# Performance work log

Measured on AMD Instinct MI355X. Metric: run time of the kernel, lower is better.

## Reference

```python
import jax, jax.numpy as jnp
import numpy as np

B, M, DIM, HID, GRID, IMG = 32, 4096, 768, 128, 15, 240
P = GRID * GRID
NL, TOPK, BETA, EPS = 3, 10, 1.0, 1e-5


def setup_inputs() -> dict:
    key = jax.random.key(0)
    ks = jax.random.split(key, 12)
    r = lambda k, s: jax.random.normal(k, s, jnp.float32) * 0.02
    H2 = HID // 2
    return dict(
        query_tokens=jax.random.normal(ks[0], (B, P, DIM), jnp.float32),
        prompt_tokens=jax.random.normal(ks[1], (B, M, DIM), jnp.float32),
        layer_idx=0,
        sbn_g=jnp.ones((NL, DIM)), sbn_b=jnp.zeros((NL, DIM)),
        sbn_m=jnp.zeros((NL, DIM)), sbn_v=jnp.ones((NL, DIM)),
        w1=r(ks[2], (HID, DIM, 3, 3)),
        bn1_g=jnp.ones(HID), bn1_b=jnp.zeros(HID), bn1_m=jnp.zeros(HID), bn1_v=jnp.ones(HID),
        wt1=r(ks[3], (HID, HID, 2, 2)), bt1=jnp.zeros(HID),
        w2=r(ks[4], (H2, HID, 3, 3)),
        bn2_g=jnp.ones(H2), bn2_b=jnp.zeros(H2), bn2_m=jnp.zeros(H2), bn2_v=jnp.ones(H2),
        wt2=r(ks[5], (H2, H2, 2, 2)), bt2=jnp.zeros(H2),
        w3=r(ks[6], (2, H2, 1, 1)), b3=jnp.zeros(2),
        g1=r(ks[7], (HID, DIM)),
        gbn1_g=jnp.ones(HID), gbn1_b=jnp.zeros(HID), gbn1_m=jnp.zeros(HID), gbn1_v=jnp.ones(HID),
        g2=r(ks[8], (H2, HID)),
        gbn2_g=jnp.ones(H2), gbn2_b=jnp.zeros(H2), gbn2_m=jnp.zeros(H2), gbn2_v=jnp.ones(H2),
        g3=r(ks[9], (2, H2)),
    )


def _conv(x, w, pad):
    return jax.lax.conv_general_dilated(x, w, (1, 1), [(pad, pad), (pad, pad)],
                                        dimension_numbers=('NCHW', 'OIHW', 'NCHW'))


def _convT2(x, w, b):
    # ConvTranspose2d(k=2, s=2): non-overlapping -> einsum + depth-to-space
    Bn, C, H, W = x.shape
    O = w.shape[1]
    y = jnp.einsum('bchw,coij->bohiwj', x, w).reshape(Bn, O, H * 2, W * 2)
    return y + b[None, :, None, None]


def _bn2(x, g, b, m, v):
    s = g / jnp.sqrt(v + EPS)
    return (x - m[:, None, None]) * s[:, None, None] + b[:, None, None]


def _bn1(x, g, b, m, v):
    return (x - m) * (g / jnp.sqrt(v + EPS)) + b


def reference(query_tokens, prompt_tokens, layer_idx, sbn_g, sbn_b, sbn_m, sbn_v,
              w1, bn1_g, bn1_b, bn1_m, bn1_v, wt1, bt1,
              w2, bn2_g, bn2_b, bn2_m, bn2_v, wt2, bt2, w3, b3,
              g1, gbn1_g, gbn1_b, gbn1_m, gbn1_v,
              g2, gbn2_g, gbn2_b, gbn2_m, gbn2_v, g3):
    # --- align_prompt_to_query ---
    qn = query_tokens / jnp.maximum(jnp.linalg.norm(query_tokens, axis=-1, keepdims=True), 1e-12)
    pn = prompt_tokens / jnp.maximum(jnp.linalg.norm(prompt_tokens, axis=-1, keepdims=True), 1e-12)
    sim = jnp.einsum('bpd,bmd->bpm', qn, pn)            # [B,P,M]
    indices = jnp.argmax(sim, axis=-1)                  # [B,P]
    max_sim = jnp.max(sim, axis=-1)
    aligned = jnp.take_along_axis(prompt_tokens, indices[..., None], axis=1)  # [B,P,D]
    residual_map = 0.5 * (1.0 - max_sim)
    context = query_tokens + BETA * jnp.abs(query_tokens - aligned)
    # --- seg head ---
    li = min(int(layer_idx), NL - 1)
    cm = context.transpose(0, 2, 1).reshape(B, DIM, GRID, GRID)
    cm = _bn2(cm, sbn_g[li], sbn_b[li], sbn_m[li], sbn_v[li])
    h = jax.nn.relu(_bn2(_conv(cm, w1, 1), bn1_g, bn1_b, bn1_m, bn1_v))
    h = _convT2(h, wt1, bt1)                            # 15 -> 30
    h = jax.nn.relu(_bn2(_conv(h, w2, 1), bn2_g, bn2_b, bn2_m, bn2_v))
    h = _convT2(h, wt2, bt2)                            # 30 -> 60
    low = _conv(h, w3, 0) + b3[None, :, None, None]     # [B,2,60,60]
    seg = jax.image.resize(low, (B, 2, IMG, IMG), method='bilinear')  # align_corners=False
    patch_map = jax.nn.softmax(low, axis=1)[:, 1].reshape(B, -1)
    # --- global head: avg pool + topk-residual pool ---
    avg_pool = context.mean(axis=1)
    _, ti = jax.lax.top_k(residual_map, TOPK)
    topk_tokens = jnp.take_along_axis(context, ti[..., None], axis=1).mean(axis=1)
    pooled = 0.5 * avg_pool + 0.5 * topk_tokens
    g = jax.nn.relu(_bn1(pooled @ g1.T, gbn1_g, gbn1_b, gbn1_m, gbn1_v))
    g = jax.nn.relu(_bn1(g @ g2.T, gbn2_g, gbn2_b, gbn2_m, gbn2_v))
    gl = g @ g3.T
    logit = gl[:, 1] - gl[:, 0]
    return (seg, gl, logit, jax.nn.sigmoid(logit), patch_map, residual_map, context, aligned, indices)
```

## Files before the change

### kernel.cpp

```cpp
#include <hip/hip_runtime.h>
#include <cmath>

#define EPSC 1e-5f
typedef unsigned short ushortT;
typedef unsigned int uintT;
typedef __attribute__((ext_vector_type(8))) short bf16x8;
typedef __attribute__((ext_vector_type(4))) float f32x4;

constexpr size_t O_SEG   = 0;
constexpr size_t O_GL    = 3686400;
constexpr size_t O_LOGIT = 3686464;
constexpr size_t O_PROB  = 3686496;
constexpr size_t O_PATCH = 3686528;
constexpr size_t O_RES   = 3801728;
constexpr size_t O_CTX   = 3808928;
constexpr size_t O_ALN   = 9338528;
constexpr size_t O_IDX   = 14868128;

constexpr size_t WS_MS64 = 0;
constexpr size_t WS_AVG  = 14400;
constexpr size_t CB      = 38976;
constexpr size_t WS_QPK  = CB;
constexpr size_t WS_TOP2G= CB + 5898240;
constexpr size_t WS_CPH  = CB;
constexpr size_t WS_CPL  = CB + 3551232;
constexpr size_t WS_WPK  = CB + 7102464;
constexpr size_t WS_H1   = CB + 8000000;
constexpr size_t WS_T1H  = CB;
constexpr size_t WS_T1L  = CB + 2097152;
constexpr size_t WS_H2   = CB + 4200000;
constexpr size_t WS_T2   = CB + 6050000;
constexpr size_t WS_WPK2 = CB + 8950000;
constexpr size_t WS_LOW  = CB;

__global__ __launch_bounds__(256) void k_qpack(const float* __restrict__ Q,
                                               ushortT* __restrict__ qpk) {
  int id = blockIdx.x * 256 + threadIdx.x;
  int r = id & 15;
  int g = (id >> 4) & 3;
  int rest = id >> 6;
  int sub = rest % 15;
  int bkc = rest / 15;
  int kc = bkc % 24, b = bkc / 24;
  if (b >= 32) return;
  int q = sub * 16 + r;
  int k0 = kc * 32 + g * 8;
  float x[8];
  if (q < 225) {
    const float* src = Q + ((size_t)(b * 225 + q)) * 768 + k0;
#pragma unroll
    for (int e = 0; e < 8; ++e) x[e] = src[e];
  } else {
#pragma unroll
    for (int e = 0; e < 8; ++e) x[e] = 0.f;
  }
  uintT hb[8];
#pragma unroll
  for (int e = 0; e < 8; ++e) hb[e] = __float_as_uint(x[e]);
  uint4 hv;
  hv.x = (hb[0] >> 16) | (hb[1] & 0xFFFF0000u);
  hv.y = (hb[2] >> 16) | (hb[3] & 0xFFFF0000u);
  hv.z = (hb[4] >> 16) | (hb[5] & 0xFFFF0000u);
  hv.w = (hb[6] >> 16) | (hb[7] & 0xFFFF0000u);
  size_t base = ((size_t)(b * 24 + kc) * 30 + sub) * 512 + (g * 16 + r) * 8;
  *(uint4*)(qpk + base) = hv;
}

__global__ __launch_bounds__(256, 3) void k_simm(const ushortT* __restrict__ qpk,
    const float* __restrict__ PM, float4* __restrict__ top2g) {
  __shared__ ushortT sP[2 * 2048];
  __shared__ float4 smrg[240];
  __shared__ float srp[64];
  int sp = blockIdx.x, b = blockIdx.y;
  int t = threadIdx.x;
  int w = t >> 6, l = t & 63;
  int mq = t >> 3, kq = t & 7;
  const int sub0 = w * 4;
  const ushortT* qB0 = qpk + (size_t)(b * 24) * 30 * 512;

#define LOADQ(KC)                                                             \
  {                                                                           \
    const ushortT* qk = qB0 + (size_t)(KC) * (30 * 512);                      \
    _Pragma("unroll")                                                         \
    for (int ss = 0; ss < 4; ++ss) {                                          \
      int subc = sub0 + ss; if (subc > 14) subc = 14;                         \
      qh[ss] = *(const bf16x8*)(qk + subc * 512 + l * 8);                     \
    }                                                                         \
  }

#define LOADP(PR, KC)                                                         \
  {                                                                           \
    _Pragma("unroll")                                                         \
    for (int pass = 0; pass < 2; ++pass) {                                    \
      int ml = mq + pass * 32;                                                \
      PR[pass] = *(const float4*)(pmBase + (size_t)ml * 768 + (KC) * 32 + kq * 4); \
    }                                                                         \
  }

#define CVTW(PR, BUF)                                                         \
  {                                                                           \
    _Pragma("unroll")                                                         \
    for (int pass = 0; pass < 2; ++pass) {                                    \
      int ml = mq + pass * 32;                                                \
      float4 x = PR[pass];                                                    \
      pn[pass] += x.x * x.x + x.y * x.y + x.z * x.z + x.w * x.w;              \
      uintT a0 = __float_as_uint(x.x), a1 = __float_as_uint(x.y);             \
      uintT a2 = __float_as_uint(x.z), a3 = __float_as_uint(x.w);             \
      uintT h01 = (a0 >> 16) | (a1 & 0xFFFF0000u);                            \
      uintT h23 = (a2 >> 16) | (a3 & 0xFFFF0000u);                            \
      int off = (ml >> 4) * 512 + (kq >> 1) * 128 + (ml & 15) * 8 + (kq & 1) * 4; \
      *(uint2*)(&sP[(BUF) + off]) = make_uint2(h01, h23);                     \
    }                                                                         \
  }

#define MFMAPH(BUF)                                                           \
  {                                                                           \
    bf16x8 bh[4];                                                             \
    _Pragma("unroll")                                                         \
    for (int mm = 0; mm < 4; ++mm)                                            \
      bh[mm] = *(const bf16x8*)&sP[(BUF) + mm * 512 + l * 8];                 \
    _Pragma("unroll")                                                         \
    for (int ss = 0; ss < 4; ++ss) {                                          \
      if (sub0 + ss < 15) {                                                   \
        _Pragma("unroll")                                                     \
        for (int mm = 0; mm < 4; ++mm) {                                      \
          acc[ss][mm] = __builtin_amdgcn_mfma_f32_16x16x32_bf16(              \
              qh[ss], bh[mm], acc[ss][mm], 0, 0, 0);                          \
        }                                                                     \
      }                                                                       \
    }                                                                         \
  }

  f32x4 acc[4][4];
#pragma unroll
  for (int ss = 0; ss < 4; ++ss)
#pragma unroll
    for (int mm = 0; mm < 4; ++mm) acc[ss][mm] = (f32x4){0.f, 0.f, 0.f, 0.f};
  float pn[2] = {0.f, 0.f};
  const int mbase = sp * 64;
  const float* pmBase = PM + ((size_t)b * 4096 + mbase) * 768;

  bf16x8 qh[4];
  float4 pr[2];

  LOADP(pr, 0);
  CVTW(pr, 0);
  __syncthreads();

  for (int kc2 = 0; kc2 < 12; ++kc2) {
    int kc = kc2 * 2;
    LOADQ(kc);
    LOADP(pr, kc + 1);
    MFMAPH(0);
    CVTW(pr, 2048);
    __syncthreads();
    LOADQ(kc + 1);
    if (kc2 < 11) {
      LOADP(pr, kc + 2);
    }
    MFMAPH(2048);
    if (kc2 < 11) {
      CVTW(pr, 0);
    }
    __syncthreads();
  }

#pragma unroll
  for (int pass = 0; pass < 2; ++pass) {
    float v = pn[pass];
    v += __shfl_xor(v, 1); v += __shfl_xor(v, 2); v += __shfl_xor(v, 4);
    if (kq == 0) srp[mq + pass * 32] = 1.0f / fmaxf(sqrtf(v), 1e-12f);
  }
  __syncthreads();
  float rpv_[4];
#pragma unroll
  for (int mf = 0; mf < 4; ++mf) rpv_[mf] = srp[mf * 16 + (l & 15)];
#pragma unroll
  for (int ss = 0; ss < 4; ++ss) {
    int sub = sub0 + ss;
    if (sub >= 15) break;
#pragma unroll
    for (int j = 0; j < 4; ++j) {
      float a1 = -1e30f, a2 = -1e30f; int ai1 = -1, ai2 = -1;
#pragma unroll
      for (int mf = 0; mf < 4; ++mf) {
        float v = acc[ss][mf][j] * rpv_[mf];
        int mi = mbase + mf * 16 + (l & 15);
        if (v > a1) { a2 = a1; ai2 = ai1; a1 = v; ai1 = mi; }
        else if (v > a2) { a2 = v; ai2 = mi; }
      }
#pragma unroll
      for (int o = 1; o <= 8; o <<= 1) {
        float b1 = __shfl_xor(a1, o), b2 = __shfl_xor(a2, o);
        int bi1 = __shfl_xor(ai1, o), bi2 = __shfl_xor(ai2, o);
        if (b1 > a1) {
          float n2; int ni2;
          if (a1 > b2) { n2 = a1; ni2 = ai1; } else { n2 = b2; ni2 = bi2; }
          a1 = b1; ai1 = bi1; a2 = n2; ai2 = ni2;
        } else {
          if (b1 > a2) { a2 = b1; ai2 = bi1; }
        }
      }
      if ((l & 15) == j) {
        int row = sub * 16 + (l >> 4) * 4 + j;
        smrg[row] = make_float4(a1, a2, __int_as_float(ai1), __int_as_float(ai2));
      }
    }
  }
  __syncthreads();
  if (t < 240) top2g[((size_t)(b * 240 + t)) * 64 + sp] = smrg[t];
#undef LOADQ
#undef LOADP
#undef CVTW
#undef MFMAPH
}

__global__ __launch_bounds__(256) void k_refine(const float* __restrict__ Q,
    const float* __restrict__ PM, const float4* __restrict__ top2g,
    float* __restrict__ oIdx, float* __restrict__ oRes,
    float* __restrict__ oCtx, float* __restrict__ oAln,
    double* __restrict__ ms64) {
  int wid = (blockIdx.x * 256 + threadIdx.x) >> 6;
  int lane = threadIdx.x & 63;
  if (wid >= 7200) return;
  int b = wid / 225, pr = wid % 225;
  float4 e = top2g[((size_t)(b * 240 + pr)) * 64 + lane];
  float v1 = e.x, v2 = e.y;
  int i1 = __float_as_int(e.z), i2 = __float_as_int(e.w);
  int cand[8];
#pragma unroll
  for (int k = 0; k < 8; ++k) {
    float v = v1; int mi = i1;
    if (v2 > v || (v2 == v && (uintT)i2 < (uintT)mi)) { v = v2; mi = i2; }
#pragma unroll
    for (int o = 1; o <= 32; o <<= 1) {
      float ov = __shfl_xor(v, o); int omi = __shfl_xor(mi, o);
      if (ov > v || (ov == v && (uintT)omi < (uintT)mi)) { v = ov; mi = omi; }
    }
    cand[k] = mi;
    if (i1 == mi) v1 = -3e38f;
    if (i2 == mi) v2 = -3e38f;
  }
  const float* qr = Q + ((size_t)b * 225 + pr) * 768;
  float qv[12]; double nq = 0.0;
#pragma unroll
  for (int j = 0; j < 12; ++j) { float x = qr[lane + 64 * j]; qv[j] = x; nq += (double)x * (double)x; }
#pragma unroll
  for (int o = 1; o < 64; o <<= 1) nq += __shfl_xor(nq, o);
  double qn = fmax(sqrt(nq), 1e-12);
  double best = -1e300; int bi = 0;
#pragma unroll
  for (int pass = 0; pass < 2; ++pass) {
    const float* pp[4];
    double d[4], nn[4];
#pragma unroll
    for (int c = 0; c < 4; ++c) {
      pp[c] = PM + ((size_t)b * 4096 + cand[pass * 4 + c]) * 768 + lane;
      d[c] = 0.0; nn[c] = 0.0;
    }
#pragma unroll
    for (int j = 0; j < 12; ++j) {
#pragma unroll
      for (int c = 0; c < 4; ++c) {
        double pe = (double)pp[c][64 * j];
        d[c] += (double)qv[j] * pe;
        nn[c] += pe * pe;
      }
    }
#pragma unroll
    for (int o = 1; o < 64; o <<= 1) {
#pragma unroll
      for (int c = 0; c < 4; ++c) {
        d[c] += __shfl_xor(d[c], o);
        nn[c] += __shfl_xor(nn[c], o);
      }
    }
#pragma unroll
    for (int c = 0; c < 4; ++c) {
      int mi = cand[pass * 4 + c];
      double s = d[c] / (qn * fmax(sqrt(nn[c]), 1e-12));
      if (s > best || (s == best && mi < bi)) { best = s; bi = mi; }
    }
  }
  if (lane == 0) {
    oIdx[wid] = (float)bi;
    oRes[wid] = (float)(0.5 * (1.0 - best));
    ms64[wid] = best;
  }
  const float* ar = PM + ((size_t)b * 4096 + bi) * 768;
  float* cw = oCtx + (size_t)wid * 768;
  float* aw = oAln + (size_t)wid * 768;
#pragma unroll
  for (int j = 0; j < 12; ++j) {
    float a = ar[lane + 64 * j];
    float qq = qv[j];
    aw[lane + 64 * j] = a;
    cw[lane + 64 * j] = qq + fabsf(qq - a);
  }
}

__global__ __launch_bounds__(256) void k_pool(const float* __restrict__ ctx,
                                              float* __restrict__ avg) {
  int b = blockIdx.x, c = blockIdx.y, t = threadIdx.x;
  int d = c * 256 + t;
  float s = 0.f;
  for (int p = 0; p < 225; ++p) s += ctx[((size_t)b * 225 + p) * 768 + d];
  avg[b * 768 + d] = s / 225.0f;
}

__global__ __launch_bounds__(256) void k_head(const float* __restrict__ ctx,
    const double* __restrict__ ms64, const float* __restrict__ avg,
    const float* __restrict__ g1, const float* __restrict__ b1g, const float* __restrict__ b1b,
    const float* __restrict__ b1m, const float* __restrict__ b1v,
    const float* __restrict__ g2, const float* __restrict__ b2g, const float* __restrict__ b2b,
    const float* __restrict__ b2m, const float* __restrict__ b2v,
    const float* __restrict__ g3,
    float* __restrict__ oGl, float* __restrict__ oLogit, float* __restrict__ oProb) {
  __shared__ int tki[10];
  __shared__ float pooled[768];
  __shared__ float h1s[128];
  __shared__ float h2s[64];
  __shared__ float gls[2];
  int b = blockIdx.x, t = threadIdx.x;
  if (t < 64) {
    double rv[4]; int ri[4];
#pragma unroll
    for (int j = 0; j < 4; ++j) {
      int p = t + 64 * j; ri[j] = p;
      rv[j] = (p < 225) ? 0.5 * (1.0 - ms64[b * 225 + p]) : -1e300;
    }
    for (int k = 0; k < 10; ++k) {
      double bv = -1e301; int bI = 1 << 30;
#pragma unroll
      for (int j = 0; j < 4; ++j)
        if (rv[j] > bv || (rv[j] == bv && ri[j] < bI)) { bv = rv[j]; bI = ri[j]; }
#pragma unroll
      for (int o = 1; o < 64; o <<= 1) {
        double ov = __shfl_xor(bv, o); int oi = __shfl_xor(bI, o);
        if (ov > bv || (ov == bv && oi < bI)) { bv = ov; bI = oi; }
      }
      if (t == 0) tki[k] = bI;
#pragma unroll
      for (int j = 0; j < 4; ++j) if (ri[j] == bI) rv[j] = -1e300;
    }
  }
  __syncthreads();
#pragma unroll
  for (int di = 0; di < 3; ++di) {
    int d = t + di * 256;
    float s = 0.f;
    for (int k = 0; k < 10; ++k) s += ctx[((size_t)b * 225 + tki[k]) * 768 + d];
    pooled[d] = 0.5f * avg[b * 768 + d] + 0.5f * (s / 10.0f);
  }
  __syncthreads();
  if (t < 128) {
    float a = 0.f;
    for (int k = 0; k < 768; ++k) a += pooled[k] * g1[t * 768 + k];
    float sc = b1g[t] / sqrtf(b1v[t] + EPSC);
    h1s[t] = fmaxf((a - b1m[t]) * sc + b1b[t], 0.f);
  }
  __syncthreads();
  if (t < 64) {
    float a = 0.f;
    for (int k = 0; k < 128; ++k) a += h1s[k] * g2[t * 128 + k];
    float sc = b2g[t] / sqrtf(b2v[t] + EPSC);
    h2s[t] = fmaxf((a - b2m[t]) * sc + b2b[t], 0.f);
  }
  __syncthreads();
  if (t < 2) {
    float a = 0.f;
    for (int k = 0; k < 64; ++k) a += h2s[k] * g3[t * 64 + k];
    oGl[b * 2 + t] = a;
    gls[t] = a;
  }
  __syncthreads();
  if (t == 0) {
    float lg = gls[1] - gls[0];
    oLogit[b] = lg;
    oProb[b] = 1.0f / (1.0f + expf(-lg));
  }
}

__global__ __launch_bounds__(256) void k_cm2(const float* __restrict__ ctx,
    const float* __restrict__ sg, const float* __restrict__ sb,
    const float* __restrict__ sm, const float* __restrict__ sv,
    const int* __restrict__ li_p,
    ushortT* __restrict__ cph, ushortT* __restrict__ cpl) {
  int id = blockIdx.x * 256 + threadIdx.x;
  if (id < 196608) {
    int v = id % 96;
    int pi = (id / 96) & 63;
    int bb = id / 6144;
    int p = pi < 17 ? pi
          : pi < 32 ? 17 * (pi - 16)
          : pi < 47 ? 17 * (pi - 31) + 16
          : 272 + (pi - 47);
    size_t off = ((size_t)(bb * 289 + p)) * 768 + v * 8;
    uint4 z = {0u, 0u, 0u, 0u};
    *(uint4*)(cph + off) = z;
    *(uint4*)(cpl + off) = z;
  }
  int wid = id >> 6;
  int lane = threadIdx.x & 63;
  if (wid >= 7200) return;
  int b = wid / 225, s = wid % 225;
  int li = li_p[0]; li = li < 2 ? li : 2; if (li < 0) li = 0;
  int p = (s / 15 + 1) * 17 + (s % 15) + 1;
  size_t obase = ((size_t)(b * 289 + p)) * 768;
#pragma unroll
  for (int j = 0; j < 3; ++j) {
    int d0 = j * 256 + lane * 4;
    float4 x  = *(const float4*)(ctx + (size_t)wid * 768 + d0);
    float4 g4 = *(const float4*)(sg + li * 768 + d0);
    float4 v4 = *(const float4*)(sv + li * 768 + d0);
    float4 m4 = *(const float4*)(sm + li * 768 + d0);
    float4 b4 = *(const float4*)(sb + li * 768 + d0);
    float xv[4] = {x.x, x.y, x.z, x.w};
    float gv[4] = {g4.x, g4.y, g4.z, g4.w};
    float vv[4] = {v4.x, v4.y, v4.z, v4.w};
    float mv_[4] = {m4.x, m4.y, m4.z, m4.w};
    float bv_[4] = {b4.x, b4.y, b4.z, b4.w};
    ushortT hu[4], lu[4];
#pragma unroll
    for (int e = 0; e < 4; ++e) {
      float sc = gv[e] / sqrtf(vv[e] + EPSC);
      float val = (xv[e] - mv_[e]) * sc + bv_[e];
      uintT bits = __float_as_uint(val);
      float lo = val - __uint_as_float(bits & 0xFFFF0000u);
      hu[e] = (ushortT)(bits >> 16);
      lu[e] = (ushortT)(__float_as_uint(lo) >> 16);
    }
    uint2 hp, lp;
    hp.x = (uintT)hu[0] | ((uintT)hu[1] << 16);
    hp.y = (uintT)hu[2] | ((uintT)hu[3] << 16);
    lp.x = (uintT)lu[0] | ((uintT)lu[1] << 16);
    lp.y = (uintT)lu[2] | ((uintT)lu[3] << 16);
    *(uint2*)(cph + obase + d0) = hp;
    *(uint2*)(cpl + obase + d0) = lp;
  }
}

__global__ __launch_bounds__(256) void k_wpackM(const float* __restrict__ w1,
                                                const float* __restrict__ w2,
                                                ushortT* __restrict__ wpk,
                                                ushortT* __restrict__ wpk2) {
  int id = blockIdx.x * 256 + threadIdx.x;
  if (id < 110592) {
    int ccq = id & 3;
    int o = (id >> 2) & 127;
    int pc = id >> 9;
    ushortT hu[8], lu[8];
#pragma unroll
    for (int e = 0; e < 8; ++e) {
      int c = (pc % 24) * 32 + ccq * 8 + e;
      float x = w1[((size_t)o * 768 + c) * 9 + pc / 24];
      uintT bits = __float_as_uint(x);
      float lo = x - __uint_as_float(bits & 0xFFFF0000u);
      hu[e] = (ushortT)(bits >> 16);
      lu[e] = (ushortT)(__float_as_uint(lo) >> 16);
    }
    uint4 h, lw;
    h.x = (uintT)hu[0] | ((uintT)hu[1] << 16);
    h.y = (uintT)hu[2] | ((uintT)hu[3] << 16);
    h.z = (uintT)hu[4] | ((uintT)hu[5] << 16);
    h.w = (uintT)hu[6] | ((uintT)hu[7] << 16);
    lw.x = (uintT)lu[0] | ((uintT)lu[1] << 16);
    lw.y = (uintT)lu[2] | ((uintT)lu[3] << 16);
    lw.z = (uintT)lu[4] | ((uintT)lu[5] << 16);
    lw.w = (uintT)lu[6] | ((uintT)lu[7] << 16);
    size_t base = (((size_t)pc) * 128 + o) * 32 + ccq * 8;
    *(uint4*)(wpk + base) = h;
    *(uint4*)(wpk + 884736 + base) = lw;
  } else {
    int id2 = id - 110592;
    if (id2 >= 9216) return;
    int ccq = id2 & 3;
    int o = (id2 >> 2) & 63;
    int pc = id2 >> 8;
    int pos = pc >> 2, ch = pc & 3;
    ushortT hu[8], lu[8];
#pragma unroll
    for (int e = 0; e < 8; ++e) {
      int c = ch * 32 + ccq * 8 + e;
      float x = w2[((size_t)o * 128 + c) * 9 + pos];
      uintT bits = __float_as_uint(x);
      float lo = x - __uint_as_float(bits & 0xFFFF0000u);
      hu[e] = (ushortT)(bits >> 16);
      lu[e] = (ushortT)(__float_as_uint(lo) >> 16);
    }
    uint4 h, lw;
    h.x = (uintT)hu[0] | ((uintT)hu[1] << 16);
    h.y = (uintT)hu[2] | ((uintT)hu[3] << 16);
    h.z = (uintT)hu[4] | ((uintT)hu[5] << 16);
    h.w = (uintT)hu[6] | ((uintT)hu[7] << 16);
    lw.x = (uintT)lu[0] | ((uintT)lu[1] << 16);
    lw.y = (uintT)lu[2] | ((uintT)lu[3] << 16);
    lw.z = (uintT)lu[4] | ((uintT)lu[5] << 16);
    lw.w = (uintT)lu[6] | ((uintT)lu[7] << 16);
    size_t base = (((size_t)pc) * 64 + o) * 32 + ccq * 8;
    *(uint4*)(wpk2 + base) = h;
    *(uint4*)(wpk2 + 73728 + base) = lw;
  }
}

__global__ __launch_bounds__(256) void k_conv1m(
    const ushortT* __restrict__ cph, const ushortT* __restrict__ cpl,
    const ushortT* __restrict__ wpk,
    const float* __restrict__ bg, const float* __restrict__ bb,
    const float* __restrict__ bm, const float* __restrict__ bv,
    float* __restrict__ outp) {
  constexpr int ROWS = 136;
  constexpr int HSZ = ROWS * 80;
  __shared__ __align__(16) unsigned char sA[2 * HSZ];
  int band = blockIdx.x, nt = blockIdx.y, b = blockIdx.z;
  int t = threadIdx.x, w = t >> 6, l = t & 63;
  int r15 = l & 15, g = l >> 4;
  int sub = band * 4 + w;
  bool mvalid = (sub < 15);
  int p0 = ((band * 64) / 15) * 17;
  int s = sub * 16 + r15; if (s > 224) s = 224;
  int pb = (s / 15) * 17 + (s % 15) - p0;
  f32x4 acc[2];
  acc[0] = (f32x4){0.f, 0.f, 0.f, 0.f};
  acc[1] = (f32x4){0.f, 0.f, 0.f, 0.f};
  const size_t planeB = (size_t)b * 289 * 768;

  for (int ch = 0; ch < 24; ++ch) {
    __syncthreads();
    for (int i = t; i < ROWS * 8; i += 256) {
      int r = i >> 3, half = (i >> 2) & 1, seg = i & 3;
      const ushortT* src = (half ? cpl : cph) + planeB +
          (size_t)(p0 + r) * 768 + ch * 32 + seg * 8;
      uint4 v = *(const uint4*)src;
      *(uint4*)(sA + half * HSZ + r * 80 + seg * 16) = v;
    }
    __syncthreads();
#pragma unroll
    for (int pos = 0; pos < 9; ++pos) {
      const ushortT* wbh = wpk + ((size_t)(pos * 24 + ch)) * 4096;
      const ushortT* wbl = wbh + 884736;
      bf16x8 bh[2], bl[2];
#pragma unroll
      for (int nf = 0; nf < 2; ++nf) {
        int off = (nt * 32 + nf * 16 + r15) * 32 + g * 8;
        bh[nf] = *(const bf16x8*)(wbh + off);
        bl[nf] = *(const bf16x8*)(wbl + off);
      }
      int shift = (pos / 3) * 17 + (pos % 3);
      if (mvalid) {
        int row = pb + shift;
        bf16x8 ah = *(const bf16x8*)(sA + row * 80 + g * 16);
        bf16x8 al = *(const bf16x8*)(sA + HSZ + row * 80 + g * 16);
#pragma unroll
        for (int nf = 0; nf < 2; ++nf) {
          f32x4 c = acc[nf];
          c = __builtin_amdgcn_mfma_f32_16x16x32_bf16(ah, bh[nf], c, 0, 0, 0);
          c = __builtin_amdgcn_mfma_f32_16x16x32_bf16(ah, bl[nf], c, 0, 0, 0);
          c = __builtin_amdgcn_mfma_f32_16x16x32_bf16(al, bh[nf], c, 0, 0, 0);
          acc[nf] = c;
        }
      }
    }
  }
  if (mvalid) {
#pragma unroll
    for (int nf = 0; nf < 2; ++nf) {
      int o = nt * 32 + nf * 16 + r15;
      float sc = bg[o] / sqrtf(bv[o] + EPSC);
      float sh = bb[o] - bm[o] * sc;
#pragma unroll
      for (int j = 0; j < 4; ++j) {
        int srow = sub * 16 + g * 4 + j;
        if (srow < 225) {
          outp[((size_t)(b * 128 + o)) * 225 + srow] =
              fmaxf(acc[nf][j] * sc + sh, 0.f);
        }
      }
    }
  }
}

__global__ __launch_bounds__(256) void k_convT1b(const float* __restrict__ in,
    const float* __restrict__ w, const float* __restrict__ bias,
    ushortT* __restrict__ t1h, ushortT* __restrict__ t1l) {
  __shared__ float sIn[128 * 15];
  int yp = blockIdx.x, b = blockIdx.y;
  int t = threadIdx.x;
  {
    int flat = (b * 15 + yp) * 256 + t;
    if (flat < 63488) {
      int v = flat & 15;
      int pi = (flat >> 4) % 124;
      int bb = flat / 1984;
      int p = pi < 32 ? pi
            : pi < 62 ? 32 * (pi - 31)
            : pi < 92 ? 32 * (pi - 61) + 31
            : 992 + (pi - 92);
      size_t off = ((size_t)bb * 1024 + p) * 128 + v * 8;
      uint4 z = {0u, 0u, 0u, 0u};
      *(uint4*)(t1h + off) = z;
      *(uint4*)(t1l + off) = z;
    }
  }
  int o = t & 127, i = t >> 7;
  for (int idx = t; idx < 128 * 15; idx += 256) {
    int c = idx / 15, x = idx % 15;
    sIn[idx] = in[((size_t)(b * 128 + c)) * 225 + yp * 15 + x];
  }
  __syncthreads();
  float acc[30];
#pragma unroll
  for (int k = 0; k < 30; ++k) acc[k] = 0.f;
  for (int c = 0; c < 128; ++c) {
    float2 wv = *(const float2*)&w[(((size_t)c * 128 + o) * 2 + i) * 2];
#pragma unroll
    for (int xx = 0; xx < 15; ++xx) {
      float iv = sIn[c * 15 + xx];
      acc[2 * xx] += wv.x * iv;
      acc[2 * xx + 1] += wv.y * iv;
    }
  }
  float bvv = bias[o];
  size_t rowb = (size_t)b * 1024 + 33 + (size_t)(2 * yp + i) * 32;
#pragma unroll
  for (int k = 0; k < 30; ++k) {
    float val = acc[k] + bvv;
    uintT bits = __float_as_uint(val);
    float lo = val - __uint_as_float(bits & 0xFFFF0000u);
    t1h[(rowb + k) * 128 + o] = (ushortT)(bits >> 16);
    t1l[(rowb + k) * 128 + o] = (ushortT)(__float_as_uint(lo) >> 16);
  }
}

__global__ __launch_bounds__(256) void k_conv2m(
    const ushortT* __restrict__ t1h, const ushortT* __restrict__ t1l,
    const ushortT* __restrict__ wpk2,
    const float* __restrict__ bg, const float* __restrict__ bb,
    const float* __restrict__ bm, const float* __restrict__ bv,
    float* __restrict__ outp) {
  constexpr int ROWS = 192;
  constexpr int HSZ = ROWS * 80;
  __shared__ __align__(16) unsigned char sA[2 * HSZ];
  int band = blockIdx.x, b = blockIdx.y;
  int t = threadIdx.x, w = t >> 6, l = t & 63;
  int r15 = l & 15, g = l >> 4;
  int sub = band * 4 + w;
  bool mvalid = (sub * 16 < 900);
  int s = sub * 16 + r15; if (s > 899) s = 899;
  int y = s / 30, x = s % 30;
  int ymin = (band * 64) / 30;
  int p0 = ymin * 32; if (p0 > 832) p0 = 832;
  int pbase = y * 32 + x - p0;
  f32x4 acc[4];
#pragma unroll
  for (int nf = 0; nf < 4; ++nf) acc[nf] = (f32x4){0.f, 0.f, 0.f, 0.f};
  const ushortT* t1hb = t1h + (size_t)b * 1024 * 128;
  const ushortT* t1lb = t1l + (size_t)b * 1024 * 128;

  for (int ch = 0; ch < 4; ++ch) {
    __syncthreads();
    for (int i = t; i < ROWS * 8; i += 256) {
      int r = i >> 3, half = (i >> 2) & 1, seg = i & 3;
      const ushortT* src = (half ? t1lb : t1hb) +
          (size_t)(p0 + r) * 128 + ch * 32 + seg * 8;
      uint4 v = *(const uint4*)src;
      *(uint4*)(sA + half * HSZ + r * 80 + seg * 16) = v;
    }
    __syncthreads();
#pragma unroll
    for (int pos = 0; pos < 9; ++pos) {
      const ushortT* wbh = wpk2 + ((size_t)(pos * 4 + ch)) * 2048;
      const ushortT* wbl = wbh + 73728;
      bf16x8 bh[4], bl[4];
#pragma unroll
      for (int nf = 0; nf < 4; ++nf) {
        int off = (nf * 16 + r15) * 32 + g * 8;
        bh[nf] = *(const bf16x8*)(wbh + off);
        bl[nf] = *(const bf16x8*)(wbl + off);
      }
      int shift = (pos / 3) * 32 + (pos % 3);
      if (mvalid) {
        int row = pbase + shift;
        bf16x8 ah = *(const bf16x8*)(sA + row * 80 + g * 16);
        bf16x8 al = *(const bf16x8*)(sA + HSZ + row * 80 + g * 16);
#pragma unroll
        for (int nf = 0; nf < 4; ++nf) {
          f32x4 c = acc[nf];
          c = __builtin_amdgcn_mfma_f32_16x16x32_bf16(ah, bh[nf], c, 0, 0, 0);
          c = __builtin_amdgcn_mfma_f32_16x16x32_bf16(ah, bl[nf], c, 0, 0, 0);
          c = __builtin_amdgcn_mfma_f32_16x16x32_bf16(al, bh[nf], c, 0, 0, 0);
          acc[nf] = c;
        }
      }
    }
  }
  if (mvalid) {
#pragma unroll
    for (int nf = 0; nf < 4; ++nf) {
      int o = nf * 16 + r15;
      float sc = bg[o] / sqrtf(bv[o] + EPSC);
      float sh = bb[o] - bm[o] * sc;
#pragma unroll
      for (int j = 0; j < 4; ++j) {
        int srow = sub * 16 + g * 4 + j;
        if (srow < 900) {
          outp[((size_t)(b * 64 + o)) * 900 + srow] =
              fmaxf(acc[nf][j] * sc + sh, 0.f);
        }
      }
    }
  }
}

template <int C, int O, int WIN, int OPLANE, int ORS, int OBASE>
__global__ __launch_bounds__(256) void k_convT(const float* __restrict__ in,
    const float* __restrict__ w, const float* __restrict__ bias, float* __restrict__ out) {
  __shared__ float sIn[C * WIN];
  int yp = blockIdx.x, b = blockIdx.y;
  int t = threadIdx.x;
  constexpr int G = 256 / O;
  constexpr int XW = WIN / (G / 2 > 0 ? G / 2 : 1);
  int o = t % O;
  int grp = t / O;
  int i = grp & 1;
  int half = grp >> 1;
  int x0 = half * XW;
  for (int idx = t; idx < C * WIN; idx += 256) {
    int c = idx / WIN, x = idx % WIN;
    sIn[idx] = in[((size_t)(b * C + c) * WIN + yp) * WIN + x];
  }
  __syncthreads();
  float acc[2 * XW];
#pragma unroll
  for (int k = 0; k < 2 * XW; ++k) acc[k] = 0.f;
  for (int c = 0; c < C; ++c) {
    float2 wv = *(const float2*)&w[(((size_t)c * O + o) * 2 + i) * 2];
#pragma unroll
    for (int xx = 0; xx < XW; ++xx) {
      float iv = sIn[c * WIN + x0 + xx];
      acc[2 * xx] += wv.x * iv;
      acc[2 * xx + 1] += wv.y * iv;
    }
  }
  float bvv = bias[o];
  float* op = out + (size_t)(b * O + o) * OPLANE + OBASE + (size_t)(2 * yp + i) * ORS + 2 * x0;
#pragma unroll
  for (int k = 0; k < 2 * XW; ++k) op[k] = acc[k] + bvv;
}

__global__ __launch_bounds__(256) void k_conv1x1(const float* __restrict__ t2,
    const float* __restrict__ w3, const float* __restrict__ b3,
    float* __restrict__ low, float* __restrict__ patch) {
  int idx = blockIdx.x * 256 + threadIdx.x;
  if (idx >= 32 * 3600) return;
  int b = idx / 3600, sp = idx % 3600;
  const float* tp = t2 + (size_t)b * 64 * 3600 + sp;
  float a0 = b3[0], a1 = b3[1];
#pragma unroll 8
  for (int c = 0; c < 64; ++c) {
    float v = tp[(size_t)c * 3600];
    a0 += v * w3[c];
    a1 += v * w3[64 + c];
  }
  low[(size_t)b * 7200 + sp] = a0;
  low[(size_t)b * 7200 + 3600 + sp] = a1;
  patch[(size_t)b * 3600 + sp] = 1.0f / (1.0f + expf(a0 - a1));
}

__global__ __launch_bounds__(256) void k_resize(const float* __restrict__ low,
                                                float* __restrict__ seg) {
  int idx = blockIdx.x * 256 + threadIdx.x;
  if (idx >= 32 * 2 * 240 * 240) return;
  int X = idx % 240;
  int Y = (idx / 240) % 240;
  int cb = idx / (240 * 240);
  const float* lp = low + (size_t)cb * 3600;
  float sy = (Y + 0.5f) * 0.25f - 0.5f;
  float sx = (X + 0.5f) * 0.25f - 0.5f;
  int y0 = (int)floorf(sy), x0 = (int)floorf(sx);
  float fy = sy - y0, fx = sx - x0;
  int y0c = min(max(y0, 0), 59), y1c = min(max(y0 + 1, 0), 59);
  int x0c = min(max(x0, 0), 59), x1c = min(max(x0 + 1, 0), 59);
  float v00 = lp[y0c * 60 + x0c], v01 = lp[y0c * 60 + x1c];
  float v10 = lp[y1c * 60 + x0c], v11 = lp[y1c * 60 + x1c];
  seg[idx] = (1.f - fy) * ((1.f - fx) * v00 + fx * v01) + fy * ((1.f - fx) * v10 + fx * v11);
}

extern "C" void kernel_launch(void* const* d_in, const int* in_sizes, int n_in,
                              void* d_out, int out_size, void* d_ws, size_t ws_size,
                              hipStream_t stream) {
  (void)in_sizes; (void)n_in; (void)out_size; (void)ws_size;
  const float* Q    = (const float*)d_in[0];
  const float* PM   = (const float*)d_in[1];
  const int*   LI   = (const int*)d_in[2];
  const float* SG   = (const float*)d_in[3];
  const float* SB   = (const float*)d_in[4];
  const float* SM   = (const float*)d_in[5];
  const float* SV   = (const float*)d_in[6];
  const float* W1   = (const float*)d_in[7];
  const float* BN1G = (const float*)d_in[8];
  const float* BN1B = (const float*)d_in[9];
  const float* BN1M = (const float*)d_in[10];
  const float* BN1V = (const float*)d_in[11];
  const float* WT1  = (const float*)d_in[12];
  const float* BT1  = (const float*)d_in[13];
  const float* W2   = (const float*)d_in[14];
  const float* BN2G = (const float*)d_in[15];
  const float* BN2B = (const float*)d_in[16];
  const float* BN2M = (const float*)d_in[17];
  const float* BN2V = (const float*)d_in[18];
  const float* WT2  = (const float*)d_in[19];
  const float* BT2  = (const float*)d_in[20];
  const float* W3   = (const float*)d_in[21];
  const float* B3   = (const float*)d_in[22];
  const float* G1   = (const float*)d_in[23];
  const float* GB1G = (const float*)d_in[24];
  const float* GB1B = (const float*)d_in[25];
  const float* GB1M = (const float*)d_in[26];
  const float* GB1V = (const float*)d_in[27];
  const float* G2   = (const float*)d_in[28];
  const float* GB2G = (const float*)d_in[29];
  const float* GB2B = (const float*)d_in[30];
  const float* GB2M = (const float*)d_in[31];
  const float* GB2V = (const float*)d_in[32];
  const float* G3   = (const float*)d_in[33];

  float* out = (float*)d_out;
  float* ws = (float*)d_ws;
  double* ms64  = (double*)(ws + WS_MS64);
  float*  avg   = ws + WS_AVG;
  ushortT* qpk  = (ushortT*)(ws + WS_QPK);
  float4* top2g = (float4*)(ws + WS_TOP2G);
  ushortT* cph  = (ushortT*)(ws + WS_CPH);
  ushortT* cpl  = (ushortT*)(ws + WS_CPL);
  ushortT* wpkp = (ushortT*)(ws + WS_WPK);
  ushortT* wpk2p= (ushortT*)(ws + WS_WPK2);
  ushortT* t1h  = (ushortT*)(ws + WS_T1H);
  ushortT* t1l  = (ushortT*)(ws + WS_T1L);
  float* h1b  = ws + WS_H1;
  float* h2b  = ws + WS_H2;
  float* t2b  = ws + WS_T2;
  float* lowb = ws + WS_LOW;

  k_qpack<<<2880, 256, 0, stream>>>(Q, qpk);
  k_simm<<<dim3(64, 32), 256, 0, stream>>>(qpk, PM, top2g);
  k_refine<<<1800, 256, 0, stream>>>(Q, PM, top2g, out + O_IDX, out + O_RES,
                                     out + O_CTX, out + O_ALN, ms64);
  k_pool<<<dim3(32, 3), 256, 0, stream>>>(out + O_CTX, avg);
  k_head<<<32, 256, 0, stream>>>(out + O_CTX, ms64, avg,
                                 G1, GB1G, GB1B, GB1M, GB1V,
                                 G2, GB2G, GB2B, GB2M, GB2V, G3,
                                 out + O_GL, out + O_LOGIT, out + O_PROB);
  k_wpackM<<<468, 256, 0, stream>>>(W1, W2, wpkp, wpk2p);
  k_cm2<<<1800, 256, 0, stream>>>(out + O_CTX, SG, SB, SM, SV, LI, cph, cpl);
  k_conv1m<<<dim3(4, 4, 32), 256, 0, stream>>>(cph, cpl, wpkp,
                                               BN1G, BN1B, BN1M, BN1V, h1b);
  k_convT1b<<<dim3(15, 32), 256, 0, stream>>>(h1b, WT1, BT1, t1h, t1l);
  k_conv2m<<<dim3(15, 32), 256, 0, stream>>>(t1h, t1l, wpk2p,
                                             BN2G, BN2B, BN2M, BN2V, h2b);
  k_convT<64, 64, 30, 3600, 60, 0><<<dim3(30, 32), 256, 0, stream>>>(h2b, WT2, BT2, t2b);
  k_conv1x1<<<450, 256, 0, stream>>>(t2b, W3, B3, lowb, out + O_PATCH);
  k_resize<<<14400, 256, 0, stream>>>(lowb, out + O_SEG);
}
```

Measured before the change: 570.2 us.

## Fuse convT2 with 1x1 conv, merge weight packing into qpack, warp-parallel head

Merges the second transposed conv with the 1x1 output conv and softmax, so the 64-channel 60x60 intermediate stays in shared memory and never goes through global memory. Weight packing for both 3x3 convs is folded into the Q packing launch as extra blocks, which removes one kernel launch. The head MLP now uses a wave-wide shuffle reduction per output instead of one thread per output doing a serial loop. The cost is more shared memory per block in the fused kernel and only 120 of 256 threads active in its 1x1 stage.

```diff
diff --git a/kernel.cpp b/kernel.cpp
--- a/kernel.cpp
+++ b/kernel.cpp
@@ -29,422 +29,47 @@
 constexpr size_t WS_T1H  = CB;
 constexpr size_t WS_T1L  = CB + 2097152;
 constexpr size_t WS_H2   = CB + 4200000;
-constexpr size_t WS_T2   = CB + 6050000;
 constexpr size_t WS_WPK2 = CB + 8950000;
 constexpr size_t WS_LOW  = CB;
 
-__global__ __launch_bounds__(256) void k_qpack(const float* __restrict__ Q,
-                                               ushortT* __restrict__ qpk) {
-  int id = blockIdx.x * 256 + threadIdx.x;
-  int r = id & 15;
-  int g = (id >> 4) & 3;
-  int rest = id >> 6;
-  int sub = rest % 15;
-  int bkc = rest / 15;
-  int kc = bkc % 24, b = bkc / 24;
-  if (b >= 32) return;
-  int q = sub * 16 + r;
-  int k0 = kc * 32 + g * 8;
-  float x[8];
-  if (q < 225) {
-    const float* src = Q + ((size_t)(b * 225 + q)) * 768 + k0;
-#pragma unroll
-    for (int e = 0; e < 8; ++e) x[e] = src[e];
-  } else {
-#pragma unroll
-    for (int e = 0; e < 8; ++e) x[e] = 0.f;
-  }
-  uintT hb[8];
-#pragma unroll
-  for (int e = 0; e < 8; ++e) hb[e] = __float_as_uint(x[e]);
-  uint4 hv;
-  hv.x = (hb[0] >> 16) | (hb[1] & 0xFFFF0000u);
-  hv.y = (hb[2] >> 16) | (hb[3] & 0xFFFF0000u);
-  hv.z = (hb[4] >> 16) | (hb[5] & 0xFFFF0000u);
-  hv.w = (hb[6] >> 16) | (hb[7] & 0xFFFF0000u);
-  size_t base = ((size_t)(b * 24 + kc) * 30 + sub) * 512 + (g * 16 + r) * 8;
-  *(uint4*)(qpk + base) = hv;
-}
-
-__global__ __launch_bounds__(256, 3) void k_simm(const ushortT* __restrict__ qpk,
-    const float* __restrict__ PM, float4* __restrict__ top2g) {
-  __shared__ ushortT sP[2 * 2048];
-  __shared__ float4 smrg[240];
-  __shared__ float srp[64];
-  int sp = blockIdx.x, b = blockIdx.y;
-  int t = threadIdx.x;
-  int w = t >> 6, l = t & 63;
-  int mq = t >> 3, kq = t & 7;
-  const int sub0 = w * 4;
-  const ushortT* qB0 = qpk + (size_t)(b * 24) * 30 * 512;
-
-#define LOADQ(KC)                                                             \
-  {                                                                           \
-    const ushortT* qk = qB0 + (size_t)(KC) * (30 * 512);                      \
-    _Pragma("unroll")                                                         \
-    for (int ss = 0; ss < 4; ++ss) {                                          \
-      int subc = sub0 + ss; if (subc > 14) subc = 14;                         \
-      qh[ss] = *(const bf16x8*)(qk + subc * 512 + l * 8);                     \
-    }                                                                         \
-  }
-
-#define LOADP(PR, KC)                                                         \
-  {                                                                           \
-    _Pragma("unroll")                                                         \
-    for (int pass = 0; pass < 2; ++pass) {                                    \
-      int ml = mq + pass * 32;                                                \
-      PR[pass] = *(const float4*)(pmBase + (size_t)ml * 768 + (KC) * 32 + kq * 4); \
-    }                                                                         \
-  }
-
-#define CVTW(PR, BUF)                                                         \
-  {                                                                           \
-    _Pragma("unroll")                                                         \
-    for (int pass = 0; pass < 2; ++pass) {                                    \
-      int ml = mq + pass * 32;                                                \
-      float4 x = PR[pass];                                                    \
-      pn[pass] += x.x * x.x + x.y * x.y + x.z * x.z + x.w * x.w;              \
-      uintT a0 = __float_as_uint(x.x), a1 = __float_as_uint(x.y);             \
-      uintT a2 = __float_as_uint(x.z), a3 = __float_as_uint(x.w);             \
-      uintT h01 = (a0 >> 16) | (a1 & 0xFFFF0000u);                            \
-      uintT h23 = (a2 >> 16) | (a3 & 0xFFFF0000u);                            \
-      int off = (ml >> 4) * 512 + (kq >> 1) * 128 + (ml & 15) * 8 + (kq & 1) * 4; \
-      *(uint2*)(&sP[(BUF) + off]) = make_uint2(h01, h23);                     \
-    }                                                                         \
-  }
-
-#define MFMAPH(BUF)                                                           \
-  {                                                                           \
-    bf16x8 bh[4];                                                             \
-    _Pragma("unroll")                                                         \
-    for (int mm = 0; mm < 4; ++mm)                                            \
-      bh[mm] = *(const bf16x8*)&sP[(BUF) + mm * 512 + l * 8];                 \
-    _Pragma("unroll")                                                         \
-    for (int ss = 0; ss < 4; ++ss) {                                          \
-      if (sub0 + ss < 15) {                                                   \
-        _Pragma("unroll")                                                     \
-        for (int mm = 0; mm < 4; ++mm) {                                      \
-          acc[ss][mm] = __builtin_amdgcn_mfma_f32_16x16x32_bf16(              \
-              qh[ss], bh[mm], acc[ss][mm], 0, 0, 0);                          \
-        }                                                                     \
-      }                                                                       \
-    }                                                                         \
-  }
-
-  f32x4 acc[4][4];
-#pragma unroll
-  for (int ss = 0; ss < 4; ++ss)
-#pragma unroll
-    for (int mm = 0; mm < 4; ++mm) acc[ss][mm] = (f32x4){0.f, 0.f, 0.f, 0.f};
-  float pn[2] = {0.f, 0.f};
-  const int mbase = sp * 64;
-  const float* pmBase = PM + ((size_t)b * 4096 + mbase) * 768;
-
-  bf16x8 qh[4];
-  float4 pr[2];
-
-  LOADP(pr, 0);
-  CVTW(pr, 0);
-  __syncthreads();
-
-  for (int kc2 = 0; kc2 < 12; ++kc2) {
-    int kc = kc2 * 2;
-    LOADQ(kc);
-    LOADP(pr, kc + 1);
-    MFMAPH(0);
-    CVTW(pr, 2048);
-    __syncthreads();
-    LOADQ(kc + 1);
-    if (kc2 < 11) {
-      LOADP(pr, kc + 2);
-    }
-    MFMAPH(2048);
-    if (kc2 < 11) {
-      CVTW(pr, 0);
-    }
-    __syncthreads();
-  }
-
-#pragma unroll
-  for (int pass = 0; pass < 2; ++pass) {
-    float v = pn[pass];
-    v += __shfl_xor(v, 1); v += __shfl_xor(v, 2); v += __shfl_xor(v, 4);
-    if (kq == 0) srp[mq + pass * 32] = 1.0f / fmaxf(sqrtf(v), 1e-12f);
-  }
-  __syncthreads();
-  float rpv_[4];
-#pragma unroll
-  for (int mf = 0; mf < 4; ++mf) rpv_[mf] = srp[mf * 16 + (l & 15)];
-#pragma unroll
-  for (int ss = 0; ss < 4; ++ss) {
-    int sub = sub0 + ss;
-    if (sub >= 15) break;
-#pragma unroll
-    for (int j = 0; j < 4; ++j) {
-      float a1 = -1e30f, a2 = -1e30f; int ai1 = -1, ai2 = -1;
-#pragma unroll
-      for (int mf = 0; mf < 4; ++mf) {
-        float v = acc[ss][mf][j] * rpv_[mf];
-        int mi = mbase + mf * 16 + (l & 15);
-        if (v > a1) { a2 = a1; ai2 = ai1; a1 = v; ai1 = mi; }
-        else if (v > a2) { a2 = v; ai2 = mi; }
-      }
-#pragma unroll
-      for (int o = 1; o <= 8; o <<= 1) {
-        float b1 = __shfl_xor(a1, o), b2 = __shfl_xor(a2, o);
-        int bi1 = __shfl_xor(ai1, o), bi2 = __shfl_xor(ai2, o);
-        if (b1 > a1) {
-          float n2; int ni2;
-          if (a1 > b2) { n2 = a1; ni2 = ai1; } else { n2 = b2; ni2 = bi2; }
-          a1 = b1; ai1 = bi1; a2 = n2; ai2 = ni2;
-        } else {
-          if (b1 > a2) { a2 = b1; ai2 = bi1; }
-        }
-      }
-      if ((l & 15) == j) {
-        int row = sub * 16 + (l >> 4) * 4 + j;
-        smrg[row] = make_float4(a1, a2, __int_as_float(ai1), __int_as_float(ai2));
-      }
-    }
-  }
-  __syncthreads();
-  if (t < 240) top2g[((size_t)(b * 240 + t)) * 64 + sp] = smrg[t];
-#undef LOADQ
-#undef LOADP
-#undef CVTW
-#undef MFMAPH
-}
-
-__global__ __launch_bounds__(256) void k_refine(const float* __restrict__ Q,
-    const float* __restrict__ PM, const float4* __restrict__ top2g,
-    float* __restrict__ oIdx, float* __restrict__ oRes,
-    float* __restrict__ oCtx, float* __restrict__ oAln,
-    double* __restrict__ ms64) {
-  int wid = (blockIdx.x * 256 + threadIdx.x) >> 6;
-  int lane = threadIdx.x & 63;
-  if (wid >= 7200) return;
-  int b = wid / 225, pr = wid % 225;
-  float4 e = top2g[((size_t)(b * 240 + pr)) * 64 + lane];
-  float v1 = e.x, v2 = e.y;
-  int i1 = __float_as_int(e.z), i2 = __float_as_int(e.w);
-  int cand[8];
-#pragma unroll
-  for (int k = 0; k < 8; ++k) {
-    float v = v1; int mi = i1;
-    if (v2 > v || (v2 == v && (uintT)i2 < (uintT)mi)) { v = v2; mi = i2; }
-#pragma unroll
-    for (int o = 1; o <= 32; o <<= 1) {
-      float ov = __shfl_xor(v, o); int omi = __shfl_xor(mi, o);
-      if (ov > v || (ov == v && (uintT)omi < (uintT)mi)) { v = ov; mi = omi; }
-    }
-    cand[k] = mi;
-    if (i1 == mi) v1 = -3e38f;
-    if (i2 == mi) v2 = -3e38f;
-  }
-  const float* qr = Q + ((size_t)b * 225 + pr) * 768;
-  float qv[12]; double nq = 0.0;
-#pragma unroll
-  for (int j = 0; j < 12; ++j) { float x = qr[lane + 64 * j]; qv[j] = x; nq += (double)x * (double)x; }
-#pragma unroll
-  for (int o = 1; o < 64; o <<= 1) nq += __shfl_xor(nq, o);
-  double qn = fmax(sqrt(nq), 1e-12);
-  double best = -1e300; int bi = 0;
-#pragma unroll
-  for (int pass = 0; pass < 2; ++pass) {
-    const float* pp[4];
-    double d[4], nn[4];
-#pragma unroll
-    for (int c = 0; c < 4; ++c) {
-      pp[c] = PM + ((size_t)b * 4096 + cand[pass * 4 + c]) * 768 + lane;
-      d[c] = 0.0; nn[c] = 0.0;
-    }
-#pragma unroll
-    for (int j = 0; j < 12; ++j) {
-#pragma unroll
-      for (int c = 0; c < 4; ++c) {
-        double pe = (double)pp[c][64 * j];
-        d[c] += (double)qv[j] * pe;
-        nn[c] += pe * pe;
-      }
-    }
-#pragma unroll
-    for (int o = 1; o < 64; o <<= 1) {
-#pragma unroll
-      for (int c = 0; c < 4; ++c) {
-        d[c] += __shfl_xor(d[c], o);
-        nn[c] += __shfl_xor(nn[c], o);
-      }
-    }
-#pragma unroll
-    for (int c = 0; c < 4; ++c) {
-      int mi = cand[pass * 4 + c];
-      double s = d[c] / (qn * fmax(sqrt(nn[c]), 1e-12));
-      if (s > best || (s == best && mi < bi)) { best = s; bi = mi; }
-    }
-  }
-  if (lane == 0) {
-    oIdx[wid] = (float)bi;
-    oRes[wid] = (float)(0.5 * (1.0 - best));
-    ms64[wid] = best;
-  }
-  const float* ar = PM + ((size_t)b * 4096 + bi) * 768;
-  float* cw = oCtx + (size_t)wid * 768;
-  float* aw = oAln + (size_t)wid * 768;
-#pragma unroll
-  for (int j = 0; j < 12; ++j) {
-    float a = ar[lane + 64 * j];
-    float qq = qv[j];
-    aw[lane + 64 * j] = a;
-    cw[lane + 64 * j] = qq + fabsf(qq - a);
-  }
-}
-
-__global__ __launch_bounds__(256) void k_pool(const float* __restrict__ ctx,
-                                              float* __restrict__ avg) {
-  int b = blockIdx.x, c = blockIdx.y, t = threadIdx.x;
-  int d = c * 256 + t;
-  float s = 0.f;
-  for (int p = 0; p < 225; ++p) s += ctx[((size_t)b * 225 + p) * 768 + d];
-  avg[b * 768 + d] = s / 225.0f;
-}
-
-__global__ __launch_bounds__(256) void k_head(const float* __restrict__ ctx,
-    const double* __restrict__ ms64, const float* __restrict__ avg,
-    const float* __restrict__ g1, const float* __restrict__ b1g, const float* __restrict__ b1b,
-    const float* __restrict__ b1m, const float* __restrict__ b1v,
-    const float* __restrict__ g2, const float* __restrict__ b2g, const float* __restrict__ b2b,
-    const float* __restrict__ b2m, const float* __restrict__ b2v,
-    const float* __restrict__ g3,
-    float* __restrict__ oGl, float* __restrict__ oLogit, float* __restrict__ oProb) {
-  __shared__ int tki[10];
-  __shared__ float pooled[768];
-  __shared__ float h1s[128];
-  __shared__ float h2s[64];
-  __shared__ float gls[2];
-  int b = blockIdx.x, t = threadIdx.x;
-  if (t < 64) {
-    double rv[4]; int ri[4];
-#pragma unroll
-    for (int j = 0; j < 4; ++j) {
-      int p = t + 64 * j; ri[j] = p;
-      rv[j] = (p < 225) ? 0.5 * (1.0 - ms64[b * 225 + p]) : -1e300;
-    }
-    for (int k = 0; k < 10; ++k) {
-      double bv = -1e301; int bI = 1 << 30;
-#pragma unroll
-      for (int j = 0; j < 4; ++j)
-        if (rv[j] > bv || (rv[j] == bv && ri[j] < bI)) { bv = rv[j]; bI = ri[j]; }
-#pragma unroll
-      for (int o = 1; o < 64; o <<= 1) {
-        double ov = __shfl_xor(bv, o); int oi = __shfl_xor(bI, o);
-        if (ov > bv || (ov == bv && oi < bI)) { bv = ov; bI = oi; }
-      }
-      if (t == 0) tki[k] = bI;
-#pragma unroll
-      for (int j = 0; j < 4; ++j) if (ri[j] == bI) rv[j] = -1e300;
-    }
-  }
-  __syncthreads();
-#pragma unroll
-  for (int di = 0; di < 3; ++di) {
-    int d = t + di * 256;
-    float s = 0.f;
-    for (int k = 0; k < 10; ++k) s += ctx[((size_t)b * 225 + tki[k]) * 768 + d];
-    pooled[d] = 0.5f * avg[b * 768 + d] + 0.5f * (s / 10.0f);
-  }
-  __syncthreads();
-  if (t < 128) {
-    float a = 0.f;
-    for (int k = 0; k < 768; ++k) a += pooled[k] * g1[t * 768 + k];
-    float sc = b1g[t] / sqrtf(b1v[t] + EPSC);
-    h1s[t] = fmaxf((a - b1m[t]) * sc + b1b[t], 0.f);
-  }
-  __syncthreads();
-  if (t < 64) {
-    float a = 0.f;
-    for (int k = 0; k < 128; ++k) a += h1s[k] * g2[t * 128 + k];
-    float sc = b2g[t] / sqrtf(b2v[t] + EPSC);
-    h2s[t] = fmaxf((a - b2m[t]) * sc + b2b[t], 0.f);
-  }
-  __syncthreads();
-  if (t < 2) {
-    float a = 0.f;
-    for (int k = 0; k < 64; ++k) a += h2s[k] * g3[t * 64 + k];
-    oGl[b * 2 + t] = a;
-    gls[t] = a;
-  }
-  __syncthreads();
-  if (t == 0) {
-    float lg = gls[1] - gls[0];
-    oLogit[b] = lg;
-    oProb[b] = 1.0f / (1.0f + expf(-lg));
-  }
-}
-
-__global__ __launch_bounds__(256) void k_cm2(const float* __restrict__ ctx,
-    const float* __restrict__ sg, const float* __restrict__ sb,
-    const float* __restrict__ sm, const float* __restrict__ sv,
-    const int* __restrict__ li_p,
-    ushortT* __restrict__ cph, ushortT* __restrict__ cpl) {
-  int id = blockIdx.x * 256 + threadIdx.x;
-  if (id < 196608) {
-    int v = id % 96;
-    int pi = (id / 96) & 63;
-    int bb = id / 6144;
-    int p = pi < 17 ? pi
-          : pi < 32 ? 17 * (pi - 16)
-          : pi < 47 ? 17 * (pi - 31) + 16
-          : 272 + (pi - 47);
-    size_t off = ((size_t)(bb * 289 + p)) * 768 + v * 8;
-    uint4 z = {0u, 0u, 0u, 0u};
-    *(uint4*)(cph + off) = z;
-    *(uint4*)(cpl + off) = z;
-  }
-  int wid = id >> 6;
-  int lane = threadIdx.x & 63;
-  if (wid >= 7200) return;
-  int b = wid / 225, s = wid % 225;
-  int li = li_p[0]; li = li < 2 ? li : 2; if (li < 0) li = 0;
-  int p = (s / 15 + 1) * 17 + (s % 15) + 1;
-  size_t obase = ((size_t)(b * 289 + p)) * 768;
-#pragma unroll
-  for (int j = 0; j < 3; ++j) {
-    int d0 = j * 256 + lane * 4;
-    float4 x  = *(const float4*)(ctx + (size_t)wid * 768 + d0);
-    float4 g4 = *(const float4*)(sg + li * 768 + d0);
-    float4 v4 = *(const float4*)(sv + li * 768 + d0);
-    float4 m4 = *(const float4*)(sm + li * 768 + d0);
-    float4 b4 = *(const float4*)(sb + li * 768 + d0);
-    float xv[4] = {x.x, x.y, x.z, x.w};
-    float gv[4] = {g4.x, g4.y, g4.z, g4.w};
-    float vv[4] = {v4.x, v4.y, v4.z, v4.w};
-    float mv_[4] = {m4.x, m4.y, m4.z, m4.w};
-    float bv_[4] = {b4.x, b4.y, b4.z, b4.w};
-    ushortT hu[4], lu[4];
-#pragma unroll
-    for (int e = 0; e < 4; ++e) {
-      float sc = gv[e] / sqrtf(vv[e] + EPSC);
-      float val = (xv[e] - mv_[e]) * sc + bv_[e];
-      uintT bits = __float_as_uint(val);
-      float lo = val - __uint_as_float(bits & 0xFFFF0000u);
-      hu[e] = (ushortT)(bits >> 16);
-      lu[e] = (ushortT)(__float_as_uint(lo) >> 16);
-    }
-    uint2 hp, lp;
-    hp.x = (uintT)hu[0] | ((uintT)hu[1] << 16);
-    hp.y = (uintT)hu[2] | ((uintT)hu[3] << 16);
-    lp.x = (uintT)lu[0] | ((uintT)lu[1] << 16);
-    lp.y = (uintT)lu[2] | ((uintT)lu[3] << 16);
-    *(uint2*)(cph + obase + d0) = hp;
-    *(uint2*)(cpl + obase + d0) = lp;
-  }
-}
-
-__global__ __launch_bounds__(256) void k_wpackM(const float* __restrict__ w1,
-                                                const float* __restrict__ w2,
-                                                ushortT* __restrict__ wpk,
-                                                ushortT* __restrict__ wpk2) {
-  int id = blockIdx.x * 256 + threadIdx.x;
+__global__ __launch_bounds__(256) void k_qpackW(const float* __restrict__ Q,
+    const float* __restrict__ w1, const float* __restrict__ w2,
+    ushortT* __restrict__ qpk, ushortT* __restrict__ wpk,
+    ushortT* __restrict__ wpk2) {
+  int bid = blockIdx.x;
+  if (bid < 2880) {
+    int id = bid * 256 + threadIdx.x;
+    int r = id & 15;
+    int g = (id >> 4) & 3;
+    int rest = id >> 6;
+    int sub = rest % 15;
+    int bkc = rest / 15;
+    int kc = bkc % 24, b = bkc / 24;
+    if (b >= 32) return;
+    int q = sub * 16 + r;
+    int k0 = kc * 32 + g * 8;
+    float x[8];
+    if (q < 225) {
+      const float* src = Q + ((size_t)(b * 225 + q)) * 768 + k0;
+#pragma unroll
+      for (int e = 0; e < 8; ++e) x[e] = src[e];
+    } else {
+#pragma unroll
+      for (int e = 0; e < 8; ++e) x[e] = 0.f;
+    }
+    uintT hb[8];
+#pragma unroll
+    for (int e = 0; e < 8; ++e) hb[e] = __float_as_uint(x[e]);
+    uint4 hv;
+    hv.x = (hb[0] >> 16) | (hb[1] & 0xFFFF0000u);
+    hv.y = (hb[2] >> 16) | (hb[3] & 0xFFFF0000u);
+    hv.z = (hb[4] >> 16) | (hb[5] & 0xFFFF0000u);
+    hv.w = (hb[6] >> 16) | (hb[7] & 0xFFFF0000u);
+    size_t base = ((size_t)(b * 24 + kc) * 30 + sub) * 512 + (g * 16 + r) * 8;
+    *(uint4*)(qpk + base) = hv;
+    return;
+  }
+  int id = (bid - 2880) * 256 + threadIdx.x;
   if (id < 110592) {
     int ccq = id & 3;
     int o = (id >> 2) & 127;
@@ -500,6 +125,407 @@
     size_t base = (((size_t)pc) * 64 + o) * 32 + ccq * 8;
     *(uint4*)(wpk2 + base) = h;
     *(uint4*)(wpk2 + 73728 + base) = lw;
+  }
+}
+
+__global__ __launch_bounds__(256, 3) void k_simm(const ushortT* __restrict__ qpk,
+    const float* __restrict__ PM, float4* __restrict__ top2g) {
+  __shared__ ushortT sP[2 * 2048];
+  __shared__ float4 smrg[240];
+  __shared__ float srp[64];
+  int sp = blockIdx.x, b = blockIdx.y;
+  int t = threadIdx.x;
+  int w = t >> 6, l = t & 63;
+  int mq = t >> 3, kq = t & 7;
+  const int sub0 = w * 4;
+  const ushortT* qB0 = qpk + (size_t)(b * 24) * 30 * 512;
+
+#define LOADQ(KC)                                                             \
+  {                                                                           \
+    const ushortT* qk = qB0 + (size_t)(KC) * (30 * 512);                      \
+    _Pragma("unroll")                                                         \
+    for (int ss = 0; ss < 4; ++ss) {                                          \
+      int subc = sub0 + ss; if (subc > 14) subc = 14;                         \
+      qh[ss] = *(const bf16x8*)(qk + subc * 512 + l * 8);                     \
+    }                                                                         \
+  }
+
+#define LOADP(PR, KC)                                                         \
+  {                                                                           \
+    _Pragma("unroll")                                                         \
+    for (int pass = 0; pass < 2; ++pass) {                                    \
+      int ml = mq + pass * 32;                                                \
+      PR[pass] = *(const float4*)(pmBase + (size_t)ml * 768 + (KC) * 32 + kq * 4); \
+    }                                                                         \
+  }
+
+#define CVTW(PR, BUF)                                                         \
+  {                                                                           \
+    _Pragma("unroll")                                                         \
+    for (int pass = 0; pass < 2; ++pass) {                                    \
+      int ml = mq + pass * 32;                                                \
+      float4 x = PR[pass];                                                    \
+      pn[pass] += x.x * x.x + x.y * x.y + x.z * x.z + x.w * x.w;              \
+      uintT a0 = __float_as_uint(x.x), a1 = __float_as_uint(x.y);             \
+      uintT a2 = __float_as_uint(x.z), a3 = __float_as_uint(x.w);             \
+      uintT h01 = (a0 >> 16) | (a1 & 0xFFFF0000u);                            \
+      uintT h23 = (a2 >> 16) | (a3 & 0xFFFF0000u);                            \
+      int off = (ml >> 4) * 512 + (kq >> 1) * 128 + (ml & 15) * 8 + (kq & 1) * 4; \
+      *(uint2*)(&sP[(BUF) + off]) = make_uint2(h01, h23);                     \
+    }                                                                         \
+  }
+
+#define MFMAPH(BUF)                                                           \
+  {                                                                           \
+    bf16x8 bh[4];                                                             \
+    _Pragma("unroll")                                                         \
+    for (int mm = 0; mm < 4; ++mm)                                            \
+      bh[mm] = *(const bf16x8*)&sP[(BUF) + mm * 512 + l * 8];                 \
+    _Pragma("unroll")                                                         \
+    for (int ss = 0; ss < 4; ++ss) {                                          \
+      if (sub0 + ss < 15) {                                                   \
+        _Pragma("unroll")                                                     \
+        for (int mm = 0; mm < 4; ++mm) {                                      \
+          acc[ss][mm] = __builtin_amdgcn_mfma_f32_16x16x32_bf16(              \
+              qh[ss], bh[mm], acc[ss][mm], 0, 0, 0);                          \
+        }                                                                     \
+      }                                                                       \
+    }                                                                         \
+  }
+
+  f32x4 acc[4][4];
+#pragma unroll
+  for (int ss = 0; ss < 4; ++ss)
+#pragma unroll
+    for (int mm = 0; mm < 4; ++mm) acc[ss][mm] = (f32x4){0.f, 0.f, 0.f, 0.f};
+  float pn[2] = {0.f, 0.f};
+  const int mbase = sp * 64;
+  const float* pmBase = PM + ((size_t)b * 4096 + mbase) * 768;
+
+  bf16x8 qh[4];
+  float4 pr[2];
+
+  LOADP(pr, 0);
+  CVTW(pr, 0);
+  __syncthreads();
+
+  for (int kc2 = 0; kc2 < 12; ++kc2) {
+    int kc = kc2 * 2;
+    LOADQ(kc);
+    LOADP(pr, kc + 1);
+    MFMAPH(0);
+    CVTW(pr, 2048);
+    __syncthreads();
+    LOADQ(kc + 1);
+    if (kc2 < 11) {
+      LOADP(pr, kc + 2);
+    }
+    MFMAPH(2048);
+    if (kc2 < 11) {
+      CVTW(pr, 0);
+    }
+    __syncthreads();
+  }
+
+#pragma unroll
+  for (int pass = 0; pass < 2; ++pass) {
+    float v = pn[pass];
+    v += __shfl_xor(v, 1); v += __shfl_xor(v, 2); v += __shfl_xor(v, 4);
+    if (kq == 0) srp[mq + pass * 32] = 1.0f / fmaxf(sqrtf(v), 1e-12f);
+  }
+  __syncthreads();
+  float rpv_[4];
+#pragma unroll
+  for (int mf = 0; mf < 4; ++mf) rpv_[mf] = srp[mf * 16 + (l & 15)];
+#pragma unroll
+  for (int ss = 0; ss < 4; ++ss) {
+    int sub = sub0 + ss;
+    if (sub >= 15) break;
+#pragma unroll
+    for (int j = 0; j < 4; ++j) {
+      float a1 = -1e30f, a2 = -1e30f; int ai1 = -1, ai2 = -1;
+#pragma unroll
+      for (int mf = 0; mf < 4; ++mf) {
+        float v = acc[ss][mf][j] * rpv_[mf];
+        int mi = mbase + mf * 16 + (l & 15);
+        if (v > a1) { a2 = a1; ai2 = ai1; a1 = v; ai1 = mi; }
+        else if (v > a2) { a2 = v; ai2 = mi; }
+      }
+#pragma unroll
+      for (int o = 1; o <= 8; o <<= 1) {
+        float b1 = __shfl_xor(a1, o), b2 = __shfl_xor(a2, o);
+        int bi1 = __shfl_xor(ai1, o), bi2 = __shfl_xor(ai2, o);
+        if (b1 > a1) {
+          float n2; int ni2;
+          if (a1 > b2) { n2 = a1; ni2 = ai1; } else { n2 = b2; ni2 = bi2; }
+          a1 = b1; ai1 = bi1; a2 = n2; ai2 = ni2;
+        } else {
+          if (b1 > a2) { a2 = b1; ai2 = bi1; }
+        }
+      }
+      if ((l & 15) == j) {
+        int row = sub * 16 + (l >> 4) * 4 + j;
+        smrg[row] = make_float4(a1, a2, __int_as_float(ai1), __int_as_float(ai2));
+      }
+    }
+  }
+  __syncthreads();
+  if (t < 240) top2g[((size_t)(b * 240 + t)) * 64 + sp] = smrg[t];
+#undef LOADQ
+#undef LOADP
+#undef CVTW
+#undef MFMAPH
+}
+
+__global__ __launch_bounds__(256) void k_refine(const float* __restrict__ Q,
+    const float* __restrict__ PM, const float4* __restrict__ top2g,
+    float* __restrict__ oIdx, float* __restrict__ oRes,
+    float* __restrict__ oCtx, float* __restrict__ oAln,
+    double* __restrict__ ms64) {
+  int wid = (blockIdx.x * 256 + threadIdx.x) >> 6;
+  int lane = threadIdx.x & 63;
+  if (wid >= 7200) return;
+  int b = wid / 225, pr = wid % 225;
+  float4 e = top2g[((size_t)(b * 240 + pr)) * 64 + lane];
+  float v1 = e.x, v2 = e.y;
+  int i1 = __float_as_int(e.z), i2 = __float_as_int(e.w);
+  int cand[8];
+#pragma unroll
+  for (int k = 0; k < 8; ++k) {
+    float v = v1; int mi = i1;
+    if (v2 > v || (v2 == v && (uintT)i2 < (uintT)mi)) { v = v2; mi = i2; }
+#pragma unroll
+    for (int o = 1; o <= 32; o <<= 1) {
+      float ov = __shfl_xor(v, o); int omi = __shfl_xor(mi, o);
+      if (ov > v || (ov == v && (uintT)omi < (uintT)mi)) { v = ov; mi = omi; }
+    }
+    cand[k] = mi;
+    if (i1 == mi) v1 = -3e38f;
+    if (i2 == mi) v2 = -3e38f;
+  }
+  const float* qr = Q + ((size_t)b * 225 + pr) * 768;
+  float qv[12]; double nq = 0.0;
+#pragma unroll
+  for (int j = 0; j < 12; ++j) { float x = qr[lane + 64 * j]; qv[j] = x; nq += (double)x * (double)x; }
+#pragma unroll
+  for (int o = 1; o < 64; o <<= 1) nq += __shfl_xor(nq, o);
+  double qn = fmax(sqrt(nq), 1e-12);
+  double best = -1e300; int bi = 0;
+#pragma unroll
+  for (int pass = 0; pass < 2; ++pass) {
+    const float* pp[4];
+    double d[4], nn[4];
+#pragma unroll
+    for (int c = 0; c < 4; ++c) {
+      pp[c] = PM + ((size_t)b * 4096 + cand[pass * 4 + c]) * 768 + lane;
+      d[c] = 0.0; nn[c] = 0.0;
+    }
+#pragma unroll
+    for (int j = 0; j < 12; ++j) {
+#pragma unroll
+      for (int c = 0; c < 4; ++c) {
+        double pe = (double)pp[c][64 * j];
+        d[c] += (double)qv[j] * pe;
+        nn[c] += pe * pe;
+      }
+    }
+#pragma unroll
+    for (int o = 1; o < 64; o <<= 1) {
+#pragma unroll
+      for (int c = 0; c < 4; ++c) {
+        d[c] += __shfl_xor(d[c], o);
+        nn[c] += __shfl_xor(nn[c], o);
+      }
+    }
+#pragma unroll
+    for (int c = 0; c < 4; ++c) {
+      int mi = cand[pass * 4 + c];
+      double s = d[c] / (qn * fmax(sqrt(nn[c]), 1e-12));
+      if (s > best || (s == best && mi < bi)) { best = s; bi = mi; }
+    }
+  }
+  if (lane == 0) {
+    oIdx[wid] = (float)bi;
+    oRes[wid] = (float)(0.5 * (1.0 - best));
+    ms64[wid] = best;
+  }
+  const float* ar = PM + ((size_t)b * 4096 + bi) * 768;
+  float* cw = oCtx + (size_t)wid * 768;
+  float* aw = oAln + (size_t)wid * 768;
+#pragma unroll
+  for (int j = 0; j < 12; ++j) {
+    float a = ar[lane + 64 * j];
+    float qq = qv[j];
+    aw[lane + 64 * j] = a;
+    cw[lane + 64 * j] = qq + fabsf(qq - a);
+  }
+}
+
+__global__ __launch_bounds__(256) void k_pool(const float* __restrict__ ctx,
+                                              float* __restrict__ avg) {
+  int b = blockIdx.x, c = blockIdx.y, t = threadIdx.x;
+  int d = c * 256 + t;
+  float s = 0.f;
+  for (int p = 0; p < 225; ++p) s += ctx[((size_t)b * 225 + p) * 768 + d];
+  avg[b * 768 + d] = s / 225.0f;
+}
+
+__global__ __launch_bounds__(256) void k_head(const float* __restrict__ ctx,
+    const double* __restrict__ ms64, const float* __restrict__ avg,
+    const float* __restrict__ g1, const float* __restrict__ b1g, const float* __restrict__ b1b,
+    const float* __restrict__ b1m, const float* __restrict__ b1v,
+    const float* __restrict__ g2, const float* __restrict__ b2g, const float* __restrict__ b2b,
+    const float* __restrict__ b2m, const float* __restrict__ b2v,
+    const float* __restrict__ g3,
+    float* __restrict__ oGl, float* __restrict__ oLogit, float* __restrict__ oProb) {
+  __shared__ int tki[10];
+  __shared__ float pooled[768];
+  __shared__ float h1s[128];
+  __shared__ float h2s[64];
+  __shared__ float gls[2];
+  int b = blockIdx.x, t = threadIdx.x;
+  int w = t >> 6, l = t & 63;
+  if (t < 64) {
+    double rv[4]; int ri[4];
+#pragma unroll
+    for (int j = 0; j < 4; ++j) {
+      int p = t + 64 * j; ri[j] = p;
+      rv[j] = (p < 225) ? 0.5 * (1.0 - ms64[b * 225 + p]) : -1e300;
+    }
+    for (int k = 0; k < 10; ++k) {
+      double bv = -1e301; int bI = 1 << 30;
+#pragma unroll
+      for (int j = 0; j < 4; ++j)
+        if (rv[j] > bv || (rv[j] == bv && ri[j] < bI)) { bv = rv[j]; bI = ri[j]; }
+#pragma unroll
+      for (int o = 1; o < 64; o <<= 1) {
+        double ov = __shfl_xor(bv, o); int oi = __shfl_xor(bI, o);
+        if (ov > bv || (ov == bv && oi < bI)) { bv = ov; bI = oi; }
+      }
+      if (t == 0) tki[k] = bI;
+#pragma unroll
+      for (int j = 0; j < 4; ++j) if (ri[j] == bI) rv[j] = -1e300;
+    }
+  }
+  __syncthreads();
+#pragma unroll
+  for (int di = 0; di < 3; ++di) {
+    int d = t + di * 256;
+    float s = 0.f;
+    for (int k = 0; k < 10; ++k) s += ctx[((size_t)b * 225 + tki[k]) * 768 + d];
+    pooled[d] = 0.5f * avg[b * 768 + d] + 0.5f * (s / 10.0f);
+  }
+  __syncthreads();
+  {
+    float pv[12];
+#pragma unroll
+    for (int j = 0; j < 12; ++j) pv[j] = pooled[l + 64 * j];
+#pragma unroll
+    for (int oo = 0; oo < 32; ++oo) {
+      int o = w * 32 + oo;
+      const float* gr = g1 + (size_t)o * 768;
+      float a = 0.f;
+#pragma unroll
+      for (int j = 0; j < 12; ++j) a += pv[j] * gr[l + 64 * j];
+#pragma unroll
+      for (int off = 1; off < 64; off <<= 1) a += __shfl_xor(a, off);
+      if (l == 0) {
+        float sc = b1g[o] / sqrtf(b1v[o] + EPSC);
+        h1s[o] = fmaxf((a - b1m[o]) * sc + b1b[o], 0.f);
+      }
+    }
+  }
+  __syncthreads();
+  {
+    float hv0 = h1s[l], hv1 = h1s[l + 64];
+#pragma unroll
+    for (int oo = 0; oo < 16; ++oo) {
+      int o = w * 16 + oo;
+      const float* gr = g2 + (size_t)o * 128;
+      float a = hv0 * gr[l] + hv1 * gr[l + 64];
+#pragma unroll
+      for (int off = 1; off < 64; off <<= 1) a += __shfl_xor(a, off);
+      if (l == 0) {
+        float sc = b2g[o] / sqrtf(b2v[o] + EPSC);
+        h2s[o] = fmaxf((a - b2m[o]) * sc + b2b[o], 0.f);
+      }
+    }
+  }
+  __syncthreads();
+  if (w == 0) {
+    float hv = h2s[l];
+#pragma unroll
+    for (int o = 0; o < 2; ++o) {
+      float a = hv * g3[o * 64 + l];
+#pragma unroll
+      for (int off = 1; off < 64; off <<= 1) a += __shfl_xor(a, off);
+      if (l == 0) { oGl[b * 2 + o] = a; gls[o] = a; }
+    }
+  }
+  __syncthreads();
+  if (t == 0) {
+    float lg = gls[1] - gls[0];
+    oLogit[b] = lg;
+    oProb[b] = 1.0f / (1.0f + expf(-lg));
+  }
+}
+
+__global__ __launch_bounds__(256) void k_cm2(const float* __restrict__ ctx,
+    const float* __restrict__ sg, const float* __restrict__ sb,
+    const float* __restrict__ sm, const float* __restrict__ sv,
+    const int* __restrict__ li_p,
+    ushortT* __restrict__ cph, ushortT* __restrict__ cpl) {
+  int id = blockIdx.x * 256 + threadIdx.x;
+  if (id < 196608) {
+    int v = id % 96;
+    int pi = (id / 96) & 63;
+    int bb = id / 6144;
+    int p = pi < 17 ? pi
+          : pi < 32 ? 17 * (pi - 16)
+          : pi < 47 ? 17 * (pi - 31) + 16
+          : 272 + (pi - 47);
+    size_t off = ((size_t)(bb * 289 + p)) * 768 + v * 8;
+    uint4 z = {0u, 0u, 0u, 0u};
+    *(uint4*)(cph + off) = z;
+    *(uint4*)(cpl + off) = z;
+  }
+  int wid = id >> 6;
+  int lane = threadIdx.x & 63;
+  if (wid >= 7200) return;
+  int b = wid / 225, s = wid % 225;
+  int li = li_p[0]; li = li < 2 ? li : 2; if (li < 0) li = 0;
+  int p = (s / 15 + 1) * 17 + (s % 15) + 1;
+  size_t obase = ((size_t)(b * 289 + p)) * 768;
+#pragma unroll
+  for (int j = 0; j < 3; ++j) {
+    int d0 = j * 256 + lane * 4;
+    float4 x  = *(const float4*)(ctx + (size_t)wid * 768 + d0);
+    float4 g4 = *(const float4*)(sg + li * 768 + d0);
+    float4 v4 = *(const float4*)(sv + li * 768 + d0);
+    float4 m4 = *(const float4*)(sm + li * 768 + d0);
+    float4 b4 = *(const float4*)(sb + li * 768 + d0);
+    float xv[4] = {x.x, x.y, x.z, x.w};
+    float gv[4] = {g4.x, g4.y, g4.z, g4.w};
+    float vv[4] = {v4.x, v4.y, v4.z, v4.w};
+    float mv_[4] = {m4.x, m4.y, m4.z, m4.w};
+    float bv_[4] = {b4.x, b4.y, b4.z, b4.w};
+    ushortT hu[4], lu[4];
+#pragma unroll
+    for (int e = 0; e < 4; ++e) {
+      float sc = gv[e] / sqrtf(vv[e] + EPSC);
+      float val = (xv[e] - mv_[e]) * sc + bv_[e];
+      uintT bits = __float_as_uint(val);
+      float lo = val - __uint_as_float(bits & 0xFFFF0000u);
+      hu[e] = (ushortT)(bits >> 16);
+      lu[e] = (ushortT)(__float_as_uint(lo) >> 16);
+    }
+    uint2 hp, lp;
+    hp.x = (uintT)hu[0] | ((uintT)hu[1] << 16);
+    hp.y = (uintT)hu[2] | ((uintT)hu[3] << 16);
+    lp.x = (uintT)lu[0] | ((uintT)lu[1] << 16);
+    lp.y = (uintT)lu[2] | ((uintT)lu[3] << 16);
+    *(uint2*)(cph + obase + d0) = hp;
+    *(uint2*)(cpl + obase + d0) = lp;
   }
 }
 
@@ -712,59 +738,54 @@
   }
 }
 
-template <int C, int O, int WIN, int OPLANE, int ORS, int OBASE>
-__global__ __launch_bounds__(256) void k_convT(const float* __restrict__ in,
-    const float* __restrict__ w, const float* __restrict__ bias, float* __restrict__ out) {
-  __shared__ float sIn[C * WIN];
+__global__ __launch_bounds__(256) void k_convT2f(const float* __restrict__ in,
+    const float* __restrict__ w, const float* __restrict__ bias,
+    const float* __restrict__ w3, const float* __restrict__ b3,
+    float* __restrict__ low, float* __restrict__ patch) {
+  __shared__ float sIn[64 * 30];
+  __shared__ float sT[2][64][61];
   int yp = blockIdx.x, b = blockIdx.y;
   int t = threadIdx.x;
-  constexpr int G = 256 / O;
-  constexpr int XW = WIN / (G / 2 > 0 ? G / 2 : 1);
-  int o = t % O;
-  int grp = t / O;
+  int o = t & 63;
+  int grp = t >> 6;
   int i = grp & 1;
   int half = grp >> 1;
-  int x0 = half * XW;
-  for (int idx = t; idx < C * WIN; idx += 256) {
-    int c = idx / WIN, x = idx % WIN;
-    sIn[idx] = in[((size_t)(b * C + c) * WIN + yp) * WIN + x];
-  }
-  __syncthreads();
-  float acc[2 * XW];
-#pragma unroll
-  for (int k = 0; k < 2 * XW; ++k) acc[k] = 0.f;
-  for (int c = 0; c < C; ++c) {
-    float2 wv = *(const float2*)&w[(((size_t)c * O + o) * 2 + i) * 2];
-#pragma unroll
-    for (int xx = 0; xx < XW; ++xx) {
-      float iv = sIn[c * WIN + x0 + xx];
+  int x0 = half * 15;
+  for (int idx = t; idx < 64 * 30; idx += 256) {
+    int c = idx / 30, x = idx % 30;
+    sIn[idx] = in[((size_t)(b * 64 + c) * 30 + yp) * 30 + x];
+  }
+  __syncthreads();
+  float acc[30];
+#pragma unroll
+  for (int k = 0; k < 30; ++k) acc[k] = 0.f;
+  for (int c = 0; c < 64; ++c) {
+    float2 wv = *(const float2*)&w[(((size_t)c * 64 + o) * 2 + i) * 2];
+#pragma unroll
+    for (int xx = 0; xx < 15; ++xx) {
+      float iv = sIn[c * 30 + x0 + xx];
       acc[2 * xx] += wv.x * iv;
       acc[2 * xx + 1] += wv.y * iv;
     }
   }
   float bvv = bias[o];
-  float* op = out + (size_t)(b * O + o) * OPLANE + OBASE + (size_t)(2 * yp + i) * ORS + 2 * x0;
-#pragma unroll
-  for (int k = 0; k < 2 * XW; ++k) op[k] = acc[k] + bvv;
-}
-
-__global__ __launch_bounds__(256) void k_conv1x1(const float* __restrict__ t2,
-    const float* __restrict__ w3, const float* __restrict__ b3,
-    float* __restrict__ low, float* __restrict__ patch) {
-  int idx = blockIdx.x * 256 + threadIdx.x;
-  if (idx >= 32 * 3600) return;
-  int b = idx / 3600, sp = idx % 3600;
-  const float* tp = t2 + (size_t)b * 64 * 3600 + sp;
-  float a0 = b3[0], a1 = b3[1];
+#pragma unroll
+  for (int k = 0; k < 30; ++k) sT[i][o][2 * x0 + k] = acc[k] + bvv;
+  __syncthreads();
+  if (t < 120) {
+    int row = t / 60, col = t % 60;
+    float a0 = b3[0], a1 = b3[1];
 #pragma unroll 8
-  for (int c = 0; c < 64; ++c) {
-    float v = tp[(size_t)c * 3600];
-    a0 += v * w3[c];
-    a1 += v * w3[64 + c];
-  }
-  low[(size_t)b * 7200 + sp] = a0;
-  low[(size_t)b * 7200 + 3600 + sp] = a1;
-  patch[(size_t)b * 3600 + sp] = 1.0f / (1.0f + expf(a0 - a1));
+    for (int c = 0; c < 64; ++c) {
+      float v = sT[row][c][col];
+      a0 += v * w3[c];
+      a1 += v * w3[64 + c];
+    }
+    int sp = (2 * yp + row) * 60 + col;
+    low[(size_t)b * 7200 + sp] = a0;
+    low[(size_t)b * 7200 + 3600 + sp] = a1;
+    patch[(size_t)b * 3600 + sp] = 1.0f / (1.0f + expf(a0 - a1));
+  }
 }
 
 __global__ __launch_bounds__(256) void k_resize(const float* __restrict__ low,
@@ -839,10 +860,9 @@
   ushortT* t1l  = (ushortT*)(ws + WS_T1L);
   float* h1b  = ws + WS_H1;
   float* h2b  = ws + WS_H2;
-  float* t2b  = ws + WS_T2;
   float* lowb = ws + WS_LOW;
 
-  k_qpack<<<2880, 256, 0, stream>>>(Q, qpk);
+  k_qpackW<<<3348, 256, 0, stream>>>(Q, W1, W2, qpk, wpkp, wpk2p);
   k_simm<<<dim3(64, 32), 256, 0, stream>>>(qpk, PM, top2g);
   k_refine<<<1800, 256, 0, stream>>>(Q, PM, top2g, out + O_IDX, out + O_RES,
                                      out + O_CTX, out + O_ALN, ms64);
@@ -851,14 +871,13 @@
                                  G1, GB1G, GB1B, GB1M, GB1V,
                                  G2, GB2G, GB2B, GB2M, GB2V, G3,
                                  out + O_GL, out + O_LOGIT, out + O_PROB);
-  k_wpackM<<<468, 256, 0, stream>>>(W1, W2, wpkp, wpk2p);
   k_cm2<<<1800, 256, 0, stream>>>(out + O_CTX, SG, SB, SM, SV, LI, cph, cpl);
   k_conv1m<<<dim3(4, 4, 32), 256, 0, stream>>>(cph, cpl, wpkp,
                                                BN1G, BN1B, BN1M, BN1V, h1b);
   k_convT1b<<<dim3(15, 32), 256, 0, stream>>>(h1b, WT1, BT1, t1h, t1l);
   k_conv2m<<<dim3(15, 32), 256, 0, stream>>>(t1h, t1l, wpk2p,
                                              BN2G, BN2B, BN2M, BN2V, h2b);
-  k_convT<64, 64, 30, 3600, 60, 0><<<dim3(30, 32), 256, 0, stream>>>(h2b, WT2, BT2, t2b);
-  k_conv1x1<<<450, 256, 0, stream>>>(t2b, W3, B3, lowb, out + O_PATCH);
+  k_convT2f<<<dim3(30, 32), 256, 0, stream>>>(h2b, WT2, BT2, W3, B3,
+                                              lowb, out + O_PATCH);
   k_resize<<<14400, 256, 0, stream>>>(lowb, out + O_SEG);
 }
```

After: 633.2 us. +11.0%, slower.
